# Performance work log

Hardware: AMD Instinct MI355X
Metric: run time of the kernel (lower is better)

## Reference

```python
import jax, jax.numpy as jnp
import numpy as np

N_NODES = 50000


def setup_inputs() -> dict:
    key = jax.random.key(0)
    ks = jax.random.split(key, 6)
    in_ch, out_ch, n_edges = 64, 64, 800000
    x = jax.random.normal(ks[0], (N_NODES, in_ch), dtype=jnp.float32)
    edge_index = jax.random.randint(ks[1], (2, n_edges), 0, N_NODES, dtype=jnp.int64)
    # Linear params (stored as [in, out] so y = x @ W + b)
    W_self = jax.random.normal(ks[2], (in_ch, out_ch), dtype=jnp.float32) / np.sqrt(in_ch)
    b_self = jax.random.normal(ks[3], (out_ch,), dtype=jnp.float32) * 0.01
    W_neigh = jax.random.normal(ks[4], (in_ch, out_ch), dtype=jnp.float32) / np.sqrt(in_ch)
    b_neigh = jax.random.normal(ks[5], (out_ch,), dtype=jnp.float32) * 0.01
    return {"x": x, "edge_index": edge_index, "W_self": W_self, "b_self": b_self,
            "W_neigh": W_neigh, "b_neigh": b_neigh}


def reference(x, edge_index, W_self, b_self, W_neigh, b_neigh):
    row, col = edge_index[0], edge_index[1]
    # project once on nodes [N, out], then gather per-edge [E, out]
    neigh_messages = x @ W_neigh + b_neigh
    aggregated = jax.ops.segment_sum(neigh_messages[row], col, num_segments=x.shape[0])
    out = x @ W_self + b_self + aggregated
    return jax.nn.relu(out)
```

## Files before the change

### kernel.cpp

```cpp
#include <hip/hip_runtime.h>
#include <hip/hip_bf16.h>

#define NN 50000
#define CH 64
#define NB 1563
#define NBLK 256


__global__ __launch_bounds__(256) void k_main(
    const int* __restrict__ rows, const int* __restrict__ cols,
    int* __restrict__ sorted, int* __restrict__ off, int E,
    const float* __restrict__ x,
    const float* __restrict__ Wself, const float* __restrict__ bself,
    const float* __restrict__ Wneigh, const float* __restrict__ bneigh,
    float* __restrict__ hout, unsigned int* __restrict__ mout)
{
    __shared__ float smem[2 * CH * CH + 32 * CH];
    __shared__ int wsum[8];
    const int tid = threadIdx.x;
    const int lane = tid & 63, wid = tid >> 6;

    if (blockIdx.x < NBLK) {
        int* lh     = (int*)smem;
        int* loff   = (int*)smem + NB;
        int* staged = (int*)smem + 2 * NB + 1;
        const int b = blockIdx.x;
        const int chunk = (E + NBLK - 1) / NBLK;
        const int beg = b * chunk;
        const int fin = min(beg + chunk, E);

        for (int k = tid; k < NB; k += 256) lh[k] = 0;
        __syncthreads();
        for (int i = beg + tid; i < fin; i += 256)
            atomicAdd(&lh[cols[i] >> 5], 1);
        __syncthreads();

        int carry = 0;
        for (int base = 0; base < NB; base += 256) {
            const int i = base + tid;
            const int v = (i < NB) ? lh[i] : 0;
            int s = v;
#pragma unroll
            for (int d = 1; d < 64; d <<= 1) {
                int t = __shfl_up(s, d);
                if (lane >= d) s += t;
            }
            if (lane == 63) wsum[wid] = s;
            __syncthreads();
            if (tid == 0) {
                int a = 0;
#pragma unroll
                for (int w = 0; w < 4; w++) { int t = wsum[w]; wsum[w] = a; a += t; }
                wsum[4] = a;
            }
            __syncthreads();
            if (i < NB) loff[i] = carry + wsum[wid] + (s - v);
            carry += wsum[4];
            __syncthreads();
        }
        if (tid == 0) loff[NB] = carry;
        __syncthreads();

        for (int k = tid; k < NB; k += 256) lh[k] = loff[k];
        __syncthreads();
        for (int i = beg + tid; i < fin; i += 256) {
            const int c = cols[i], r = rows[i];
            const int pos = atomicAdd(&lh[c >> 5], 1);
            staged[pos] = ((c & 31) << 16) | r;
        }
        __syncthreads();
        const int cnt = fin - beg;
        for (int i = tid; i < cnt; i += 256) sorted[beg + i] = staged[i];
        for (int k = tid; k < NB + 1; k += 256) off[b * (NB + 1) + k] = loff[k];
        return;
    }

    float* ws = smem;
    float* wn = smem + CH * CH;
    float* xs = smem + 2 * CH * CH;
    const int node0 = (blockIdx.x - NBLK) * 32;

    for (int i = tid * 4; i < CH * CH; i += 256 * 4) {
        *(float4*)&ws[i] = *(const float4*)&Wself[i];
        *(float4*)&wn[i] = *(const float4*)&Wneigh[i];
    }
    for (int i = tid * 4; i < 32 * CH; i += 256 * 4) {
        const int nd = node0 + (i >> 6);
        float4 v = {0.f, 0.f, 0.f, 0.f};
        if (nd < NN) v = *(const float4*)&x[(size_t)nd * CH + (i & 63)];
        *(float4*)&xs[i] = v;
    }
    __syncthreads();

    const int r0 = wid * 8;
    const float bsv = bself[lane];
    const float bnv = bneigh[lane];

    float accs[8], accn[8];
#pragma unroll
    for (int n = 0; n < 8; n++) { accs[n] = bsv; accn[n] = bnv; }

#pragma unroll 1
    for (int k4 = 0; k4 < CH; k4 += 4) {
        float4 xv[8];
#pragma unroll
        for (int n = 0; n < 8; n++)
            xv[n] = *(const float4*)&xs[(r0 + n) * CH + k4];
#pragma unroll
        for (int j = 0; j < 4; j++) {
            const float wsk = ws[(k4 + j) * CH + lane];
            const float wnk = wn[(k4 + j) * CH + lane];
#pragma unroll
            for (int n = 0; n < 8; n++) {
                const float xj = (j == 0) ? xv[n].x : (j == 1) ? xv[n].y
                               : (j == 2) ? xv[n].z : xv[n].w;
                accs[n] = fmaf(xj, wsk, accs[n]);
                accn[n] = fmaf(xj, wnk, accn[n]);
            }
        }
    }

#pragma unroll
    for (int n = 0; n < 8; n++) {
        const int nd = node0 + r0 + n;
        const float partner = __shfl_xor(accn[n], 1);
        if (nd < NN) {
            hout[(size_t)nd * CH + lane] = accs[n];
            if ((lane & 1) == 0) {
                __hip_bfloat162 p;
                p.x = __float2bfloat16(accn[n]);
                p.y = __float2bfloat16(partner);
                mout[(size_t)nd * 32 + (lane >> 1)] =
                    *reinterpret_cast<unsigned int*>(&p);
            }
        }
    }
}

__global__ __launch_bounds__(512) void k_gfin3(
    const unsigned int* __restrict__ mb, const int* __restrict__ off,
    const int* __restrict__ sorted, float* __restrict__ out, int E)
{
    __shared__ int pairs[4096];
    __shared__ unsigned short srcs[4096];
    __shared__ int segoff[257];
    __shared__ int fh[32], foff[33], fcur[32];
    __shared__ int wsum[8];

    const int g = blockIdx.x;
    const int tid = threadIdx.x;
    const int lane = tid & 63, wave = tid >> 6;
    const int chunk = (E + NBLK - 1) / NBLK;

    int s0 = 0, mycnt = 0;
    if (tid < 256) {
        s0    = off[tid * (NB + 1) + g];
        mycnt = off[tid * (NB + 1) + g + 1] - s0;
    }
    {
        int s = mycnt;
#pragma unroll
        for (int d = 1; d < 64; d <<= 1) {
            int t = __shfl_up(s, d);
            if (lane >= d) s += t;
        }
        if (tid < 256 && lane == 63) wsum[wave] = s;
        __syncthreads();
        if (tid == 0) {
            int a = 0;
#pragma unroll
            for (int w = 0; w < 4; w++) { int t = wsum[w]; wsum[w] = a; a += t; }
            wsum[4] = a;
        }
        __syncthreads();
        if (tid < 256) {
            const int myoff = wsum[wave] + (s - mycnt);
            segoff[tid] = myoff;
            const int src = tid * chunk + s0;
            for (int j = 0; j < mycnt; j++) {
                const int dst = myoff + j;
                if (dst < 4096) pairs[dst] = sorted[src + j];
            }
        }
        if (tid == 0) segoff[256] = wsum[4];
    }
    __syncthreads();
    const int cn = min(segoff[256], 4096);

    if (tid < 32) fh[tid] = 0;
    __syncthreads();
    for (int i = tid; i < cn; i += 512)
        atomicAdd(&fh[pairs[i] >> 16], 1);
    __syncthreads();
    if (tid < 64) {
        const int v = (lane < 32) ? fh[lane] : 0;
        int s = v;
#pragma unroll
        for (int d = 1; d < 32; d <<= 1) {
            int t = __shfl_up(s, d);
            if (lane >= d) s += t;
        }
        if (lane < 32) { foff[lane] = s - v; fcur[lane] = s - v; }
        if (lane == 0) foff[32] = cn;
    }
    __syncthreads();
    for (int i = tid; i < cn; i += 512) {
        const int p = pairs[i];
        const int pos = atomicAdd(&fcur[p >> 16], 1);
        srcs[pos] = (unsigned short)(p & 0xFFFF);
    }
    __syncthreads();

    const int c2 = lane & 31;
    const int half = lane >> 5;
    float accL[4], accH[4];
#pragma unroll
    for (int r = 0; r < 4; r++) { accL[r] = 0.f; accH[r] = 0.f; }

#pragma unroll
    for (int r = 0; r < 4; r++) {
        const int nl = wave * 4 + r;
        const int j0 = foff[nl], j1 = foff[nl + 1];
        float l0 = 0.f, l1 = 0.f, l2 = 0.f, l3 = 0.f;
        float h0 = 0.f, h1 = 0.f, h2 = 0.f, h3 = 0.f;
        int j = j0 + half;
        for (; j + 6 < j1; j += 8) {
            const unsigned int v0 = mb[(int)srcs[j]     * 32 + c2];
            const unsigned int v1 = mb[(int)srcs[j + 2] * 32 + c2];
            const unsigned int v2 = mb[(int)srcs[j + 4] * 32 + c2];
            const unsigned int v3 = mb[(int)srcs[j + 6] * 32 + c2];
            l0 += __uint_as_float(v0 << 16); h0 += __uint_as_float(v0 & 0xFFFF0000u);
            l1 += __uint_as_float(v1 << 16); h1 += __uint_as_float(v1 & 0xFFFF0000u);
            l2 += __uint_as_float(v2 << 16); h2 += __uint_as_float(v2 & 0xFFFF0000u);
            l3 += __uint_as_float(v3 << 16); h3 += __uint_as_float(v3 & 0xFFFF0000u);
        }
        for (; j < j1; j += 2) {
            const unsigned int v = mb[(int)srcs[j] * 32 + c2];
            l0 += __uint_as_float(v << 16); h0 += __uint_as_float(v & 0xFFFF0000u);
        }
        accL[r] += (l0 + l1) + (l2 + l3);
        accH[r] += (h0 + h1) + (h2 + h3);
    }

#pragma unroll
    for (int r = 0; r < 4; r++) {
        accL[r] += __shfl_xor(accL[r], 32);
        accH[r] += __shfl_xor(accH[r], 32);
        const int nd = g * 32 + wave * 4 + r;
        if (nd < NN) {
            const int o = nd * CH + 2 * c2 + half;
            const float myv = half ? accH[r] : accL[r];
            out[o] = fmaxf(out[o] + myv, 0.f);
        }
    }
}

extern "C" void kernel_launch(void* const* d_in, const int* in_sizes, int n_in,
                              void* d_out, int out_size, void* d_ws, size_t ws_size,
                              hipStream_t stream)
{
    const float* x      = (const float*)d_in[0];
    const int*   edges  = (const int*)d_in[1];
    const float* Wself  = (const float*)d_in[2];
    const float* bself  = (const float*)d_in[3];
    const float* Wneigh = (const float*)d_in[4];
    const float* bneigh = (const float*)d_in[5];
    float* out = (float*)d_out;

    const int E = in_sizes[1] / 2;
    const int* rows = edges;
    const int* cols = edges + E;

    char* ws_base = (char*)d_ws;
    unsigned int* msgb = (unsigned int*)(ws_base);
    int*   sorted = (int*)(ws_base + 12800000);
    int*   off    = (int*)(ws_base + 16000000);

    const int bP = (NN + 31) / 32;
    k_main<<<NBLK + bP, 256, 0, stream>>>(rows, cols, sorted, off, E,
                                          x, Wself, bself, Wneigh, bneigh,
                                          out, msgb);
    k_gfin3<<<NB, 512, 0, stream>>>(msgb, off, sorted, out, E);
}
```

Baseline: 59.50 us.

## Compute node projections with bf16 MFMA using prepacked weight fragments

```diff
diff --git a/kernel.cpp b/kernel.cpp
--- a/kernel.cpp
+++ b/kernel.cpp
@@ -6,24 +6,53 @@
 #define NB 1563
 #define NBLK 256
 
+typedef __attribute__((ext_vector_type(8))) short short8;
+typedef __attribute__((ext_vector_type(4))) float f32x4;
+
+__device__ __forceinline__ unsigned short f2bf(float f) {
+    __hip_bfloat16 h = __float2bfloat16(f);
+    return *reinterpret_cast<unsigned short*>(&h);
+}
+
+
+__global__ __launch_bounds__(128) void k_prep(
+    const float* __restrict__ Ws, const float* __restrict__ Wn,
+    uint4* __restrict__ wfrag)
+{
+    const int ni = blockIdx.x;
+    const int t  = threadIdx.x;
+    const int ks = t >> 6, l = t & 63;
+    const int c16 = l & 15, kg = l >> 4;
+    const int k0 = ks * 32 + kg * 8;
+    const float* B = (ni < 4) ? Ws : Wn;
+    const int c = ((ni < 4) ? ni : ni - 4) * 16 + c16;
+    unsigned int w4[4];
+#pragma unroll
+    for (int jj = 0; jj < 4; jj++) {
+        const unsigned short lo = f2bf(B[(k0 + 2 * jj)     * CH + c]);
+        const unsigned short hi = f2bf(B[(k0 + 2 * jj + 1) * CH + c]);
+        w4[jj] = (unsigned int)lo | ((unsigned int)hi << 16);
+    }
+    wfrag[(ni * 2 + ks) * 64 + l] = make_uint4(w4[0], w4[1], w4[2], w4[3]);
+}
 
 __global__ __launch_bounds__(256) void k_main(
     const int* __restrict__ rows, const int* __restrict__ cols,
     int* __restrict__ sorted, int* __restrict__ off, int E,
     const float* __restrict__ x,
-    const float* __restrict__ Wself, const float* __restrict__ bself,
-    const float* __restrict__ Wneigh, const float* __restrict__ bneigh,
+    const float* __restrict__ bself, const float* __restrict__ bneigh,
+    const short8* __restrict__ wfrag,
     float* __restrict__ hout, unsigned int* __restrict__ mout)
 {
-    __shared__ float smem[2 * CH * CH + 32 * CH];
+    __shared__ int smem[2 * NB + 1 + 3200];
     __shared__ int wsum[8];
     const int tid = threadIdx.x;
     const int lane = tid & 63, wid = tid >> 6;
 
     if (blockIdx.x < NBLK) {
-        int* lh     = (int*)smem;
-        int* loff   = (int*)smem + NB;
-        int* staged = (int*)smem + 2 * NB + 1;
+        int* lh     = smem;
+        int* loff   = smem + NB;
+        int* staged = smem + 2 * NB + 1;
         const int b = blockIdx.x;
         const int chunk = (E + NBLK - 1) / NBLK;
         const int beg = b * chunk;
@@ -75,63 +104,59 @@
         return;
     }
 
-    float* ws = smem;
-    float* wn = smem + CH * CH;
-    float* xs = smem + 2 * CH * CH;
     const int node0 = (blockIdx.x - NBLK) * 32;
-
-    for (int i = tid * 4; i < CH * CH; i += 256 * 4) {
-        *(float4*)&ws[i] = *(const float4*)&Wself[i];
-        *(float4*)&wn[i] = *(const float4*)&Wneigh[i];
-    }
-    for (int i = tid * 4; i < 32 * CH; i += 256 * 4) {
-        const int nd = node0 + (i >> 6);
-        float4 v = {0.f, 0.f, 0.f, 0.f};
-        if (nd < NN) v = *(const float4*)&x[(size_t)nd * CH + (i & 63)];
-        *(float4*)&xs[i] = v;
-    }
-    __syncthreads();
-
-    const int r0 = wid * 8;
-    const float bsv = bself[lane];
-    const float bnv = bneigh[lane];
-
-    float accs[8], accn[8];
-#pragma unroll
-    for (int n = 0; n < 8; n++) { accs[n] = bsv; accn[n] = bnv; }
-
-#pragma unroll 1
-    for (int k4 = 0; k4 < CH; k4 += 4) {
-        float4 xv[8];
-#pragma unroll
-        for (int n = 0; n < 8; n++)
-            xv[n] = *(const float4*)&xs[(r0 + n) * CH + k4];
-#pragma unroll
-        for (int j = 0; j < 4; j++) {
-            const float wsk = ws[(k4 + j) * CH + lane];
-            const float wnk = wn[(k4 + j) * CH + lane];
-#pragma unroll
-            for (int n = 0; n < 8; n++) {
-                const float xj = (j == 0) ? xv[n].x : (j == 1) ? xv[n].y
-                               : (j == 2) ? xv[n].z : xv[n].w;
-                accs[n] = fmaf(xj, wsk, accs[n]);
-                accn[n] = fmaf(xj, wnk, accn[n]);
-            }
-        }
-    }
-
-#pragma unroll
-    for (int n = 0; n < 8; n++) {
-        const int nd = node0 + r0 + n;
-        const float partner = __shfl_xor(accn[n], 1);
-        if (nd < NN) {
-            hout[(size_t)nd * CH + lane] = accs[n];
-            if ((lane & 1) == 0) {
-                __hip_bfloat162 p;
-                p.x = __float2bfloat16(accn[n]);
-                p.y = __float2bfloat16(partner);
-                mout[(size_t)nd * 32 + (lane >> 1)] =
-                    *reinterpret_cast<unsigned int*>(&p);
+    const int mi = wid & 1;
+    const int niBase = (wid >> 1) * 4;
+    const int c16 = lane & 15, kg = lane >> 4;
+
+    int arow = node0 + mi * 16 + c16;
+    if (arow > NN - 1) arow = NN - 1;
+    const size_t abase = (size_t)arow * CH;
+    short8 af[2];
+#pragma unroll
+    for (int ks = 0; ks < 2; ks++) {
+        const float4 p = *(const float4*)&x[abase + ks * 32 + kg * 8];
+        const float4 q = *(const float4*)&x[abase + ks * 32 + kg * 8 + 4];
+        short8 a;
+        a[0] = (short)f2bf(p.x); a[1] = (short)f2bf(p.y);
+        a[2] = (short)f2bf(p.z); a[3] = (short)f2bf(p.w);
+        a[4] = (short)f2bf(q.x); a[5] = (short)f2bf(q.y);
+        a[6] = (short)f2bf(q.z); a[7] = (short)f2bf(q.w);
+        af[ks] = a;
+    }
+
+    f32x4 acc[4];
+#pragma unroll
+    for (int t2 = 0; t2 < 4; t2++) {
+        const int ni = niBase + t2;
+        const float bias = (ni < 4) ? bself[ni * 16 + c16]
+                                    : bneigh[(ni - 4) * 16 + c16];
+        acc[t2] = (f32x4){bias, bias, bias, bias};
+#pragma unroll
+        for (int ks = 0; ks < 2; ks++) {
+            const short8 bf = wfrag[(ni * 2 + ks) * 64 + lane];
+            acc[t2] = __builtin_amdgcn_mfma_f32_16x16x32_bf16(af[ks], bf,
+                                                              acc[t2], 0, 0, 0);
+        }
+    }
+
+#pragma unroll
+    for (int t2 = 0; t2 < 4; t2++) {
+        const int ni = niBase + t2;
+#pragma unroll
+        for (int r = 0; r < 4; r++) {
+            const int node = node0 + mi * 16 + kg * 4 + r;
+            const float v = acc[t2][r];
+            if (ni < 4) {
+                if (node < NN)
+                    hout[(size_t)node * CH + ni * 16 + c16] = v;
+            } else {
+                const float partner = __shfl_xor(v, 1);
+                if (node < NN && (lane & 1) == 0) {
+                    const unsigned int pk = (unsigned int)f2bf(v)
+                                          | ((unsigned int)f2bf(partner) << 16);
+                    mout[(size_t)node * 32 + (ni - 4) * 8 + (c16 >> 1)] = pk;
+                }
             }
         }
     }
@@ -275,10 +300,13 @@
     unsigned int* msgb = (unsigned int*)(ws_base);
     int*   sorted = (int*)(ws_base + 12800000);
     int*   off    = (int*)(ws_base + 16000000);
+    uint4* wfrag  = (uint4*)(ws_base + 17700000);
+
+    k_prep<<<8, 128, 0, stream>>>(Wself, Wneigh, wfrag);
 
     const int bP = (NN + 31) / 32;
     k_main<<<NBLK + bP, 256, 0, stream>>>(rows, cols, sorted, off, E,
-                                          x, Wself, bself, Wneigh, bneigh,
-                                          out, msgb);
+                                          x, bself, bneigh,
+                                          (const short8*)wfrag, out, msgb);
     k_gfin3<<<NB, 512, 0, stream>>>(msgb, off, sorted, out, E);
 }
```

Result: no change. 58.51 us (-1.7%).
